# Performance work log

Measured on AMD Instinct MI355X. Metric: run time of the kernel, lower is better.

The kernel has to match this reference:

```python
import jax, jax.numpy as jnp
import numpy as np


def setup_inputs() -> dict:
    key = jax.random.key(0)
    k1, k2, k3, k4 = jax.random.split(key, 4)
    B, S, K, R, DIN, DOUT = 8, 2048, 16, 16, 2048, 2048
    h = jax.random.normal(k1, (B, S, DIN), dtype=jnp.float32)
    alpha = jax.random.uniform(k2, (B, K), dtype=jnp.float32)
    A_bank = jax.random.normal(k3, (K, R, DIN), dtype=jnp.float32) * (1.0 / np.sqrt(DIN))
    B_bank = jax.random.normal(k4, (K, DOUT, R), dtype=jnp.float32) * (1.0 / np.sqrt(R))
    return {"h": h, "alpha": alpha, "A_bank": A_bank, "B_bank": B_bank}


def reference(h, alpha, A_bank, B_bank):
    # Mix K low-rank bases per sample, then apply low-rank delta to h.
    A_mixed = jnp.einsum('bk,kri->bri', alpha, A_bank)   # [B, r, d_in]
    B_mixed = jnp.einsum('bk,kor->bor', alpha, B_bank)   # [B, d_out, r]
    z = jnp.einsum('bri,bsi->bsr', A_mixed, h)           # [B, S, r]
    delta = jnp.einsum('bor,bsr->bso', B_mixed, z)       # [B, S, d_out]
    return delta
```

## Files before the change

### kernel.cpp

```cpp
#include <hip/hip_runtime.h>

typedef unsigned int u32;
typedef float f32x4 __attribute__((ext_vector_type(4)));

#define BB 8
#define SS 2048
#define KK 16
#define RR 16
#define DIN 2048
#define DOUT 2048

__global__ void __launch_bounds__(256) mix_kernel(
    const float* __restrict__ alpha,
    const float* __restrict__ A_bank,
    const float* __restrict__ B_bank,
    float* __restrict__ Am,
    float* __restrict__ Bm)
{
    int t = blockIdx.x * 256 + threadIdx.x;
    const int half = BB * RR * DIN;
    if (t < half) {
        int i = t & (DIN - 1);
        int r = (t >> 11) & (RR - 1);
        int b = t >> 15;
        float acc = 0.f;
#pragma unroll
        for (int k = 0; k < KK; ++k)
            acc += alpha[b * KK + k] * A_bank[(k * RR + r) * DIN + i];
        Am[t] = acc;
    } else {
        int u = t - half;
        int r = u & (RR - 1);
        int o = (u >> 4) & (DOUT - 1);
        int b = u >> 15;
        float acc = 0.f;
#pragma unroll
        for (int k = 0; k < KK; ++k)
            acc += alpha[b * KK + k] * B_bank[(k * DOUT + o) * RR + r];
        Bm[u] = acc;
    }
}

__global__ void __launch_bounds__(256, 3) fused_kernel(
    const float* __restrict__ h,
    const float* __restrict__ Am,
    const float* __restrict__ Bm,
    float* __restrict__ out)
{
    __shared__ float zt[16 * 16];

    int b = blockIdx.y;
    int wid = threadIdx.x >> 6;
    int lane = threadIdx.x & 63;
    int s0 = blockIdx.x * 16;
    int sw = s0 + wid * 4;

    const float* hb = h + (size_t)b * SS * DIN + (size_t)sw * DIN;
    const float* Ab = Am + (size_t)b * RR * DIN;

    float a[64];
#pragma unroll
    for (int v = 0; v < 64; ++v) a[v] = 0.f;

#pragma unroll 1
    for (int t = 0; t < 8; ++t) {
        int i0 = t * 256 + lane * 4;
        f32x4 hv0 = __builtin_nontemporal_load((const f32x4*)(hb + i0));
        f32x4 hv1 = __builtin_nontemporal_load((const f32x4*)(hb + DIN + i0));
        f32x4 hv2 = __builtin_nontemporal_load((const f32x4*)(hb + 2 * DIN + i0));
        f32x4 hv3 = __builtin_nontemporal_load((const f32x4*)(hb + 3 * DIN + i0));
#pragma unroll
        for (int r = 0; r < 16; ++r) {
            f32x4 av = *(const f32x4*)(Ab + r * DIN + i0);
            a[0 * 16 + r] += hv0.x * av.x + hv0.y * av.y + hv0.z * av.z + hv0.w * av.w;
            a[1 * 16 + r] += hv1.x * av.x + hv1.y * av.y + hv1.z * av.z + hv1.w * av.w;
            a[2 * 16 + r] += hv2.x * av.x + hv2.y * av.y + hv2.z * av.z + hv2.w * av.w;
            a[3 * 16 + r] += hv3.x * av.x + hv3.y * av.y + hv3.z * av.z + hv3.w * av.w;
        }
    }

#pragma unroll
    for (int off = 32; off >= 1; off >>= 1) {
        bool up = (lane & off) != 0;
#pragma unroll
        for (int v = 0; v < off; ++v) {
            float send = up ? a[v] : a[v + off];
            float keep = up ? a[v + off] : a[v];
            a[v] = keep + __shfl_xor(send, off, 64);
        }
    }
    zt[wid * 64 + lane] = a[0];
    __syncthreads();

    float* op = out + ((size_t)b * SS + s0) * DOUT;

#pragma unroll 1
    for (int oc = 0; oc < 2; ++oc) {
        int o0 = oc * 1024 + threadIdx.x * 4;
        const float* wp = Bm + ((size_t)b * DOUT + o0) * RR;
        float w[4][16];
#pragma unroll
        for (int j = 0; j < 4; ++j) {
#pragma unroll
            for (int q = 0; q < 4; ++q) {
                f32x4 p = *(const f32x4*)(wp + j * RR + q * 4);
                w[j][q * 4 + 0] = p.x; w[j][q * 4 + 1] = p.y;
                w[j][q * 4 + 2] = p.z; w[j][q * 4 + 3] = p.w;
            }
        }
#pragma unroll 4
        for (int s = 0; s < 16; ++s) {
            float zz[16];
#pragma unroll
            for (int q = 0; q < 4; ++q) {
                f32x4 zv = *(const f32x4*)(zt + s * 16 + q * 4);
                zz[q * 4 + 0] = zv.x; zz[q * 4 + 1] = zv.y;
                zz[q * 4 + 2] = zv.z; zz[q * 4 + 3] = zv.w;
            }
            float rj[4];
#pragma unroll
            for (int j = 0; j < 4; ++j) {
                float acc = 0.f;
#pragma unroll
                for (int r = 0; r < 16; ++r) acc += w[j][r] * zz[r];
                rj[j] = acc;
            }
            f32x4 res;
            res.x = rj[0]; res.y = rj[1]; res.z = rj[2]; res.w = rj[3];
            __builtin_nontemporal_store(res, (f32x4*)(op + (size_t)s * DOUT + o0));
        }
    }
}

extern "C" void kernel_launch(void* const* d_in, const int* in_sizes, int n_in,
                              void* d_out, int out_size, void* d_ws, size_t ws_size,
                              hipStream_t stream)
{
    const float* h      = (const float*)d_in[0];
    const float* alpha  = (const float*)d_in[1];
    const float* A_bank = (const float*)d_in[2];
    const float* B_bank = (const float*)d_in[3];
    float* out = (float*)d_out;

    float* Am = (float*)d_ws;
    float* Bm = Am + BB * RR * DIN;

    mix_kernel<<<2048, 256, 0, stream>>>(alpha, A_bank, B_bank, Am, Bm);
    fused_kernel<<<dim3(128, 8), 256, 0, stream>>>(h, Am, Bm, out);
}
```

Before: 259.6 us.

## Stage mixed A chunks into LDS with double-buffered global_load_lds

Before this change each of the four waves in a block loaded the same 16x256 slice of the mixed A matrix from global memory (L2/L1) on every chunk. Now the block cooperatively copies each slice into shared memory with direct global-to-LDS loads, double-buffered so the next chunk's copy overlaps the current chunk's dot products. The cost is 32KB of LDS per block, which may limit occupancy, plus a block-wide barrier per chunk.

```diff
diff --git a/kernel.cpp b/kernel.cpp
--- a/kernel.cpp
+++ b/kernel.cpp
@@ -1,6 +1,5 @@
 #include <hip/hip_runtime.h>
 
-typedef unsigned int u32;
 typedef float f32x4 __attribute__((ext_vector_type(4)));
 
 #define BB 8
@@ -41,12 +40,20 @@
     }
 }
 
+__device__ __forceinline__ void stage16(const float* g, float* l)
+{
+    __builtin_amdgcn_global_load_lds(
+        (const __attribute__((address_space(1))) void*)g,
+        (__attribute__((address_space(3))) void*)l, 16, 0, 0);
+}
+
 __global__ void __launch_bounds__(256, 3) fused_kernel(
     const float* __restrict__ h,
     const float* __restrict__ Am,
     const float* __restrict__ Bm,
     float* __restrict__ out)
 {
+    __shared__ float As[2][16][256];
     __shared__ float zt[16 * 16];
 
     int b = blockIdx.y;
@@ -62,21 +69,38 @@
 #pragma unroll
     for (int v = 0; v < 64; ++v) a[v] = 0.f;
 
+#pragma unroll
+    for (int q = 0; q < 4; ++q) {
+        int r = wid * 4 + q;
+        stage16(Ab + (size_t)r * DIN + lane * 4, &As[0][r][0]);
+    }
+    __syncthreads();
+
 #pragma unroll 1
-    for (int t = 0; t < 8; ++t) {
-        int i0 = t * 256 + lane * 4;
+    for (int c = 0; c < 8; ++c) {
+        if (c < 7) {
+#pragma unroll
+            for (int q = 0; q < 4; ++q) {
+                int r = wid * 4 + q;
+                stage16(Ab + (size_t)r * DIN + (c + 1) * 256 + lane * 4,
+                        &As[(c + 1) & 1][r][0]);
+            }
+        }
+        int i0 = c * 256 + lane * 4;
         f32x4 hv0 = __builtin_nontemporal_load((const f32x4*)(hb + i0));
         f32x4 hv1 = __builtin_nontemporal_load((const f32x4*)(hb + DIN + i0));
         f32x4 hv2 = __builtin_nontemporal_load((const f32x4*)(hb + 2 * DIN + i0));
         f32x4 hv3 = __builtin_nontemporal_load((const f32x4*)(hb + 3 * DIN + i0));
+        const float (*Ac)[256] = As[c & 1];
 #pragma unroll
         for (int r = 0; r < 16; ++r) {
-            f32x4 av = *(const f32x4*)(Ab + r * DIN + i0);
+            f32x4 av = *(const f32x4*)(&Ac[r][lane * 4]);
             a[0 * 16 + r] += hv0.x * av.x + hv0.y * av.y + hv0.z * av.z + hv0.w * av.w;
             a[1 * 16 + r] += hv1.x * av.x + hv1.y * av.y + hv1.z * av.z + hv1.w * av.w;
             a[2 * 16 + r] += hv2.x * av.x + hv2.y * av.y + hv2.z * av.z + hv2.w * av.w;
             a[3 * 16 + r] += hv3.x * av.x + hv3.y * av.y + hv3.z * av.z + hv3.w * av.w;
         }
+        __syncthreads();
     }
 
 #pragma unroll
```

Result: faster. 247.9 us (-4.5%).
